# Optimization experiments

Hardware: AMD Instinct MI355X
Metric: run time of the kernel (lower is better)

Reference implementation:

```python
import jax, jax.numpy as jnp
import numpy as np

N_NODES = 500000
N_GRAPHS = 10000
NIN = 128
NOUT = 128
EPS = 1e-5


def setup_inputs() -> dict:
    key = jax.random.key(0)
    ks = jax.random.split(key, 10)
    x = jax.random.normal(ks[0], (N_NODES, NIN), dtype=jnp.float32)
    edge_index = jax.random.randint(ks[1], (2, 1000), 0, N_NODES, dtype=jnp.int64)
    edge_attr = jax.random.normal(ks[2], (1000, NIN), dtype=jnp.float32)
    batch = jnp.sort(jax.random.randint(ks[3], (N_NODES,), 0, N_GRAPHS, dtype=jnp.int64))
    s = 1.0 / np.sqrt(NIN)
    W_lin = jax.random.uniform(ks[4], (NIN, NIN), jnp.float32, -s, s)  # Linear(nin, nin, bias=False)
    bn_g = jnp.ones((NIN,), jnp.float32)
    bn_b = jnp.zeros((NIN,), jnp.float32)
    # MLP(nin, nout, nlayer=2, with_final_activation=False): Lin->BN->ReLU->Lin
    W1 = jax.random.uniform(ks[5], (NIN, NOUT), jnp.float32, -s, s)
    b1 = jax.random.uniform(ks[6], (NOUT,), jnp.float32, -s, s)
    bn1_g = jnp.ones((NOUT,), jnp.float32)
    bn1_b = jnp.zeros((NOUT,), jnp.float32)
    so = 1.0 / np.sqrt(NOUT)
    W2 = jax.random.uniform(ks[7], (NOUT, NOUT), jnp.float32, -so, so)
    b2 = jax.random.uniform(ks[8], (NOUT,), jnp.float32, -so, so)
    return {"x": x, "edge_index": edge_index, "edge_attr": edge_attr, "batch": batch,
            "W_lin": W_lin, "bn_g": bn_g, "bn_b": bn_b,
            "W1": W1, "b1": b1, "bn1_g": bn1_g, "bn1_b": bn1_b, "W2": W2, "b2": b2}


def _batchnorm(v, g, b):
    # training-mode BatchNorm1d: biased variance over dim 0
    mu = jnp.mean(v, axis=0, keepdims=True)
    var = jnp.mean(jnp.square(v - mu), axis=0, keepdims=True)
    return (v - mu) * jax.lax.rsqrt(var + EPS) * g + b


def reference(x, edge_index, edge_attr, batch, W_lin, bn_g, bn_b, W1, b1, bn1_g, bn1_b, W2, b2):
    # scatter-sum pooling: [num_graphs, nin]
    summation = jax.ops.segment_sum(x, batch, num_segments=N_GRAPHS)
    summation = summation @ W_lin.T if False else summation @ W_lin  # stored as [in,out]
    summation = jax.nn.relu(_batchnorm(summation, bn_g, bn_b))
    h = x + summation[batch]  # gather-broadcast add back to nodes
    # 2-layer MLP, no final activation
    h = jax.nn.relu(_batchnorm(h @ W1 + b1, bn1_g, bn1_b))
    return h @ W2 + b2
```

## Files before the change

### kernel.cpp

```cpp
#include <hip/hip_runtime.h>
#include <hip/hip_bf16.h>
#include <cstdint>
#include <cstddef>

#define NN 500000
#define NG 10000
#define F  128
#define EPSV 1e-5f

typedef __attribute__((ext_vector_type(8))) short short8;
typedef __attribute__((ext_vector_type(4))) float floatx4;

__device__ __forceinline__ short bfs(float f) {
    __hip_bfloat16 h = __float2bfloat16(f);
    union { __hip_bfloat16 h; unsigned short u; } c; c.h = h;
    return (short)c.u;
}
__device__ __forceinline__ int getb(const int* __restrict__ b, int i, int is64) {
    return is64 ? b[2 * i] : b[i];
}

__global__ void k_detect(const int* __restrict__ batch, int* __restrict__ flag) {
    __shared__ int nz;
    if (threadIdx.x == 0) nz = 0;
    __syncthreads();
    int j = 100001 + threadIdx.x * 1500;
    if (batch[j] != 0) atomicAdd(&nz, 1);
    __syncthreads();
    if (threadIdx.x == 0) flag[0] = (nz == 0) ? 1 : 0;
}

__global__ void k_bounds(const int* __restrict__ batch, int* __restrict__ gs, int* __restrict__ ge,
                         const int* __restrict__ flag) {
    int is64 = flag[0];
    int i = blockIdx.x * 256 + threadIdx.x;
    if (i >= NN) return;
    int b = getb(batch, i, is64);
    if (i == 0      || getb(batch, i - 1, is64) != b) gs[b] = i;
    if (i == NN - 1 || getb(batch, i + 1, is64) != b) ge[b] = i + 1;
}

__global__ void k_segsum(const float* __restrict__ x, const int* __restrict__ gs,
                         const int* __restrict__ ge, float* __restrict__ S,
                         unsigned short* __restrict__ xb) {
    __shared__ float red[8][128];
    int g = blockIdx.x;
    int s = gs[g], e = ge[g];
    int o = threadIdx.x & 31, rl = threadIdx.x >> 5;
    float acc[4] = {0.f, 0.f, 0.f, 0.f};
    for (int r = s + rl; r < e; r += 8) {
        float4 v = *reinterpret_cast<const float4*>(x + (size_t)r * F + o * 4);
        acc[0] += v.x; acc[1] += v.y; acc[2] += v.z; acc[3] += v.w;
        if (xb) {
            ushort4 bv;
            bv.x = (unsigned short)bfs(v.x); bv.y = (unsigned short)bfs(v.y);
            bv.z = (unsigned short)bfs(v.z); bv.w = (unsigned short)bfs(v.w);
            *reinterpret_cast<ushort4*>(xb + (size_t)r * F + o * 4) = bv;
        }
    }
#pragma unroll
    for (int j = 0; j < 4; j++) red[rl][o * 4 + j] = acc[j];
    __syncthreads();
    if (threadIdx.x < 128) {
        float ssum = 0.f;
#pragma unroll
        for (int rr = 0; rr < 8; rr++) ssum += red[rr][threadIdx.x];
        S[(size_t)g * F + threadIdx.x] = ssum;
    }
}

__global__ void k_wfrag(const float* __restrict__ W1, const float* __restrict__ W2,
                        unsigned short* __restrict__ W1f, unsigned short* __restrict__ W2f) {
    int i = blockIdx.x * 256 + threadIdx.x;
    int sel = i >> 14, j = i & 16383;
    int n = j >> 7, kk = j & 127;
    const float* W = sel ? W2 : W1;
    unsigned short* Wf = sel ? W2f : W1f;
    Wf[j] = (unsigned short)bfs(W[kk * F + n]);
}

__global__ void k_rowmm(const float* __restrict__ A, const float* __restrict__ W,
                        const float* __restrict__ bias, float* __restrict__ out, int hasBias) {
    int r = blockIdx.x * 2 + (threadIdx.x >> 7);
    int c = threadIdx.x & 127;
    const float* a = A + (size_t)r * F;
    float acc = hasBias ? bias[c] : 0.f;
#pragma unroll 4
    for (int k = 0; k < F; k++) acc += a[k] * W[k * F + c];
    out[(size_t)r * F + c] = acc;
}

__global__ void k_colstats(const float* __restrict__ T, float* __restrict__ sum, float* __restrict__ sumsq) {
    int f = threadIdx.x;
    int lo = blockIdx.x * 157;
    int hi = lo + 157; if (hi > NG) hi = NG;
    float s = 0.f, q = 0.f;
    for (int r = lo; r < hi; r++) { float v = T[(size_t)r * F + f]; s += v; q += v * v; }
    atomicAdd(&sum[f], s); atomicAdd(&sumsq[f], q);
}

__global__ void k_bn0(const float* __restrict__ sum, const float* __restrict__ sumsq,
                      const float* __restrict__ g, const float* __restrict__ b,
                      float* __restrict__ scale, float* __restrict__ shift) {
    int f = threadIdx.x;
    float mu  = sum[f] / (float)NG;
    float var = sumsq[f] / (float)NG - mu * mu;
    float rs  = rsqrtf(var + EPSV);
    float sc  = g[f] * rs;
    scale[f] = sc; shift[f] = b[f] - mu * sc;
}

__global__ void k_bnrelu(const float* __restrict__ T, const float* __restrict__ scale,
                         const float* __restrict__ shift, float* __restrict__ S2) {
    int e = (blockIdx.x * 256 + threadIdx.x) * 4;
    float4 t = *reinterpret_cast<const float4*>(T + e);
    int c = e & 127;
    float4 o;
    o.x = fmaxf(t.x * scale[c]     + shift[c],     0.f);
    o.y = fmaxf(t.y * scale[c + 1] + shift[c + 1], 0.f);
    o.z = fmaxf(t.z * scale[c + 2] + shift[c + 2], 0.f);
    o.w = fmaxf(t.w * scale[c + 3] + shift[c + 3], 0.f);
    *reinterpret_cast<float4*>(S2 + e) = o;
}

__device__ __forceinline__ short8 ld8bf(const float* __restrict__ p) {
    float4 f0 = *reinterpret_cast<const float4*>(p);
    float4 f1 = *reinterpret_cast<const float4*>(p + 4);
    short8 r;
    r[0] = bfs(f0.x); r[1] = bfs(f0.y); r[2] = bfs(f0.z); r[3] = bfs(f0.w);
    r[4] = bfs(f1.x); r[5] = bfs(f1.y); r[6] = bfs(f1.z); r[7] = bfs(f1.w);
    return r;
}


__global__ __launch_bounds__(256, 4)
void k_pass1(const unsigned short* __restrict__ xb, const int* __restrict__ batch,
             const unsigned short* __restrict__ W1f, const float* __restrict__ Z,
             float* __restrict__ partials, const int* __restrict__ flag) {
    const int is64 = flag[0];
    const int lane = threadIdx.x & 63;
    const int wave = threadIdx.x >> 6;
    const int wm = wave & 1, wn = wave >> 1;
    const int quad = lane >> 4, l16 = lane & 15;

    const unsigned short* wbase = W1f + ((wn * 64 + l16) * F + quad * 8);

    float su[4], sq[4];
#pragma unroll
    for (int nt = 0; nt < 4; nt++) { su[nt] = 0.f; sq[nt] = 0.f; }

    const int NT = (NN + 63) / 64;
    for (int tile = blockIdx.x; tile < NT; tile += gridDim.x) {
        int rb = tile * 64 + wm * 32;
        floatx4 acc[2][4];
#pragma unroll
        for (int mt = 0; mt < 2; mt++)
#pragma unroll
            for (int nt = 0; nt < 4; nt++) acc[mt][nt] = (floatx4){0.f, 0.f, 0.f, 0.f};

#pragma unroll
        for (int kt = 0; kt < 4; kt++) {
            short8 A[2];
#pragma unroll
            for (int mt = 0; mt < 2; mt++) {
                int r = rb + mt * 16 + l16; if (r >= NN) r = NN - 1;
                A[mt] = *reinterpret_cast<const short8*>(xb + (size_t)r * F + kt * 32 + quad * 8);
            }
#pragma unroll
            for (int nt = 0; nt < 4; nt++) {
                short8 B = *reinterpret_cast<const short8*>(wbase + nt * 16 * F + kt * 32);
#pragma unroll
                for (int mt = 0; mt < 2; mt++)
                    acc[mt][nt] = __builtin_amdgcn_mfma_f32_16x16x32_bf16(A[mt], B, acc[mt][nt], 0, 0, 0);
            }
        }

#pragma unroll
        for (int mt = 0; mt < 2; mt++)
#pragma unroll
            for (int reg = 0; reg < 4; reg++) {
                int r = rb + mt * 16 + quad * 4 + reg;
                bool valid = r < NN;
                int g = getb(batch, valid ? r : NN - 1, is64);
                const float* zr = Z + (size_t)g * F + wn * 64 + l16;
#pragma unroll
                for (int nt = 0; nt < 4; nt++) {
                    float u = acc[mt][nt][reg] + zr[nt * 16];
                    if (valid) { su[nt] += u; sq[nt] += u * u; }
                }
            }
    }

    float* ps = partials + (size_t)(blockIdx.x & 63) * 256;
#pragma unroll
    for (int nt = 0; nt < 4; nt++) {
        float s = su[nt], q = sq[nt];
        s += __shfl_xor(s, 16, 64); s += __shfl_xor(s, 32, 64);
        q += __shfl_xor(q, 16, 64); q += __shfl_xor(q, 32, 64);
        if (quad == 0) {
            int col = wn * 64 + nt * 16 + l16;
            atomicAdd(&ps[col], s);
            atomicAdd(&ps[128 + col], q);
        }
    }
}

__global__ void k_bn1(const float* __restrict__ partials, const float* __restrict__ g1,
                      const float* __restrict__ b1g, float* __restrict__ scale1,
                      float* __restrict__ shift1) {
    int f = threadIdx.x;
    float s = 0.f, q = 0.f;
    for (int t = 0; t < 64; t++) { s += partials[t * 256 + f]; q += partials[t * 256 + 128 + f]; }
    float mu  = s / (float)NN;
    float var = q / (float)NN - mu * mu;
    float rs  = rsqrtf(var + EPSV);
    float sc  = g1[f] * rs;
    scale1[f] = sc; shift1[f] = b1g[f] - mu * sc;
}

__global__ __launch_bounds__(256, 4)
void k_pass2(const unsigned short* __restrict__ xb, const int* __restrict__ batch,
             const unsigned short* W1f, const unsigned short* W2f,
             const float* __restrict__ Z, const float* __restrict__ scale1,
             const float* __restrict__ shift1, const float* __restrict__ b2,
             float* out, const int* __restrict__ flag) {
    __shared__ unsigned short h2[2][64][136];
    const int is64 = flag[0];
    const int lane = threadIdx.x & 63;
    const int wave = threadIdx.x >> 6;
    const int wm = wave & 1, wn = wave >> 1;
    const int quad = lane >> 4, l16 = lane & 15;

    float sc1[4], sh1[4], bb2[4];
#pragma unroll
    for (int nt = 0; nt < 4; nt++) {
        int n = wn * 64 + nt * 16 + l16;
        sc1[nt] = scale1[n]; sh1[nt] = shift1[n]; bb2[nt] = b2[n];
    }
    const unsigned short* w1base = W1f + ((wn * 64 + l16) * F + quad * 8);
    const unsigned short* w2base = W2f + ((wn * 64 + l16) * F + quad * 8);

    int buf = 0;
    const int NT = (NN + 63) / 64;
    for (int tile = blockIdx.x; tile < NT; tile += gridDim.x) {
        int rb = tile * 64 + wm * 32;
        floatx4 acc[2][4];
#pragma unroll
        for (int mt = 0; mt < 2; mt++)
#pragma unroll
            for (int nt = 0; nt < 4; nt++) acc[mt][nt] = (floatx4){0.f, 0.f, 0.f, 0.f};

#pragma unroll
        for (int kt = 0; kt < 4; kt++) {
            short8 A[2];
#pragma unroll
            for (int mt = 0; mt < 2; mt++) {
                int r = rb + mt * 16 + l16; if (r >= NN) r = NN - 1;
                A[mt] = *reinterpret_cast<const short8*>(xb + (size_t)r * F + kt * 32 + quad * 8);
            }
#pragma unroll
            for (int nt = 0; nt < 4; nt++) {
                short8 B = *reinterpret_cast<const short8*>(w1base + nt * 16 * F + kt * 32);
#pragma unroll
                for (int mt = 0; mt < 2; mt++)
                    acc[mt][nt] = __builtin_amdgcn_mfma_f32_16x16x32_bf16(A[mt], B, acc[mt][nt], 0, 0, 0);
            }
        }

#pragma unroll
        for (int mt = 0; mt < 2; mt++)
#pragma unroll
            for (int reg = 0; reg < 4; reg++) {
                int lr = wm * 32 + mt * 16 + quad * 4 + reg;
                int r = tile * 64 + lr; if (r >= NN) r = NN - 1;
                int g = getb(batch, r, is64);
                const float* zr = Z + (size_t)g * F + wn * 64 + l16;
#pragma unroll
                for (int nt = 0; nt < 4; nt++) {
                    float u = acc[mt][nt][reg] + zr[nt * 16];
                    float h = fmaxf(u * sc1[nt] + sh1[nt], 0.f);
                    h2[buf][lr][wn * 64 + nt * 16 + l16] = (unsigned short)bfs(h);
                }
            }
        __syncthreads();

        floatx4 acc2[2][4];
#pragma unroll
        for (int mt = 0; mt < 2; mt++)
#pragma unroll
            for (int nt = 0; nt < 4; nt++) acc2[mt][nt] = (floatx4){0.f, 0.f, 0.f, 0.f};
#pragma unroll
        for (int kt = 0; kt < 4; kt++) {
            short8 A2[2];
#pragma unroll
            for (int mt = 0; mt < 2; mt++)
                A2[mt] = *reinterpret_cast<const short8*>(&h2[buf][wm * 32 + mt * 16 + l16][kt * 32 + quad * 8]);
#pragma unroll
            for (int nt = 0; nt < 4; nt++) {
                short8 B = *reinterpret_cast<const short8*>(w2base + nt * 16 * F + kt * 32);
#pragma unroll
                for (int mt = 0; mt < 2; mt++)
                    acc2[mt][nt] = __builtin_amdgcn_mfma_f32_16x16x32_bf16(A2[mt], B, acc2[mt][nt], 0, 0, 0);
            }
        }

#pragma unroll
        for (int mt = 0; mt < 2; mt++)
#pragma unroll
            for (int reg = 0; reg < 4; reg++) {
                int r = rb + mt * 16 + quad * 4 + reg;
                if (r < NN) {
#pragma unroll
                    for (int nt = 0; nt < 4; nt++)
                        out[(size_t)r * F + wn * 64 + nt * 16 + l16] = acc2[mt][nt][reg] + bb2[nt];
                }
            }
        buf ^= 1;
    }
}


__global__ __launch_bounds__(256, 2)
void k_pass1_old(const float* __restrict__ x, const int* __restrict__ batch,
                 const float* __restrict__ W1, const float* __restrict__ Z,
                 float* __restrict__ partials, const int* __restrict__ flag) {
    const int is64 = flag[0];
    const int lane = threadIdx.x & 63;
    const int wave = threadIdx.x >> 6;
    const int wm = wave & 1, wn = wave >> 1;
    const int quad = lane >> 4, l16 = lane & 15;

    short8 Bf[4][4];
#pragma unroll
    for (int nt = 0; nt < 4; nt++) {
        int n = wn * 64 + nt * 16 + l16;
#pragma unroll
        for (int kt = 0; kt < 4; kt++)
#pragma unroll
            for (int j = 0; j < 8; j++)
                Bf[nt][kt][j] = bfs(W1[(kt * 32 + quad * 8 + j) * F + n]);
    }

    float su[4], sq[4];
#pragma unroll
    for (int nt = 0; nt < 4; nt++) { su[nt] = 0.f; sq[nt] = 0.f; }

    const int NT = (NN + 63) / 64;
    for (int tile = blockIdx.x; tile < NT; tile += gridDim.x) {
        int rb = tile * 64 + wm * 32;
        floatx4 acc[2][4];
#pragma unroll
        for (int mt = 0; mt < 2; mt++)
#pragma unroll
            for (int nt = 0; nt < 4; nt++) acc[mt][nt] = (floatx4){0.f, 0.f, 0.f, 0.f};

#pragma unroll
        for (int kt = 0; kt < 4; kt++) {
            short8 A[2];
#pragma unroll
            for (int mt = 0; mt < 2; mt++) {
                int r = rb + mt * 16 + l16; if (r >= NN) r = NN - 1;
                A[mt] = ld8bf(x + (size_t)r * F + kt * 32 + quad * 8);
            }
#pragma unroll
            for (int mt = 0; mt < 2; mt++)
#pragma unroll
                for (int nt = 0; nt < 4; nt++)
                    acc[mt][nt] = __builtin_amdgcn_mfma_f32_16x16x32_bf16(A[mt], Bf[nt][kt], acc[mt][nt], 0, 0, 0);
        }

#pragma unroll
        for (int mt = 0; mt < 2; mt++)
#pragma unroll
            for (int reg = 0; reg < 4; reg++) {
                int r = rb + mt * 16 + quad * 4 + reg;
                bool valid = r < NN;
                int g = getb(batch, valid ? r : NN - 1, is64);
                const float* zr = Z + (size_t)g * F + wn * 64 + l16;
#pragma unroll
                for (int nt = 0; nt < 4; nt++) {
                    float u = acc[mt][nt][reg] + zr[nt * 16];
                    if (valid) { su[nt] += u; sq[nt] += u * u; }
                }
            }
    }

    float* ps = partials + (size_t)(blockIdx.x & 63) * 256;
#pragma unroll
    for (int nt = 0; nt < 4; nt++) {
        float s = su[nt], q = sq[nt];
        s += __shfl_xor(s, 16, 64); s += __shfl_xor(s, 32, 64);
        q += __shfl_xor(q, 16, 64); q += __shfl_xor(q, 32, 64);
        if (quad == 0) {
            int col = wn * 64 + nt * 16 + l16;
            atomicAdd(&ps[col], s);
            atomicAdd(&ps[128 + col], q);
        }
    }
}

__global__ __launch_bounds__(256, 2)
void k_pass2_old(const float* __restrict__ x, const int* __restrict__ batch,
                 const float* __restrict__ W1, const float* __restrict__ W2,
                 const float* __restrict__ Z, const float* __restrict__ scale1,
                 const float* __restrict__ shift1, const float* __restrict__ b2,
                 float* __restrict__ out, const int* __restrict__ flag) {
    extern __shared__ unsigned short h2[];
    const int is64 = flag[0];
    const int lane = threadIdx.x & 63;
    const int wave = threadIdx.x >> 6;
    const int wm = wave & 1, wn = wave >> 1;
    const int quad = lane >> 4, l16 = lane & 15;

    short8 Bf1[4][4], Bf2[4][4];
    float sc1[4], sh1[4], bb2[4];
#pragma unroll
    for (int nt = 0; nt < 4; nt++) {
        int n = wn * 64 + nt * 16 + l16;
        sc1[nt] = scale1[n]; sh1[nt] = shift1[n]; bb2[nt] = b2[n];
#pragma unroll
        for (int kt = 0; kt < 4; kt++)
#pragma unroll
            for (int j = 0; j < 8; j++) {
                int k = kt * 32 + quad * 8 + j;
                Bf1[nt][kt][j] = bfs(W1[k * F + n]);
                Bf2[nt][kt][j] = bfs(W2[k * F + n]);
            }
    }

    const int NT = (NN + 63) / 64;
    for (int tile = blockIdx.x; tile < NT; tile += gridDim.x) {
        int rb = tile * 64 + wm * 32;
        floatx4 acc[2][4];
#pragma unroll
        for (int mt = 0; mt < 2; mt++)
#pragma unroll
            for (int nt = 0; nt < 4; nt++) acc[mt][nt] = (floatx4){0.f, 0.f, 0.f, 0.f};

#pragma unroll
        for (int kt = 0; kt < 4; kt++) {
            short8 A[2];
#pragma unroll
            for (int mt = 0; mt < 2; mt++) {
                int r = rb + mt * 16 + l16; if (r >= NN) r = NN - 1;
                A[mt] = ld8bf(x + (size_t)r * F + kt * 32 + quad * 8);
            }
#pragma unroll
            for (int mt = 0; mt < 2; mt++)
#pragma unroll
                for (int nt = 0; nt < 4; nt++)
                    acc[mt][nt] = __builtin_amdgcn_mfma_f32_16x16x32_bf16(A[mt], Bf1[nt][kt], acc[mt][nt], 0, 0, 0);
        }

        __syncthreads();
#pragma unroll
        for (int mt = 0; mt < 2; mt++)
#pragma unroll
            for (int reg = 0; reg < 4; reg++) {
                int lr = wm * 32 + mt * 16 + quad * 4 + reg;
                int r = tile * 64 + lr; if (r >= NN) r = NN - 1;
                int g = getb(batch, r, is64);
                const float* zr = Z + (size_t)g * F + wn * 64 + l16;
#pragma unroll
                for (int nt = 0; nt < 4; nt++) {
                    float u = acc[mt][nt][reg] + zr[nt * 16];
                    float h = fmaxf(u * sc1[nt] + sh1[nt], 0.f);
                    h2[lr * 136 + wn * 64 + nt * 16 + l16] = (unsigned short)bfs(h);
                }
            }
        __syncthreads();

        floatx4 acc2[2][4];
#pragma unroll
        for (int mt = 0; mt < 2; mt++)
#pragma unroll
            for (int nt = 0; nt < 4; nt++) acc2[mt][nt] = (floatx4){0.f, 0.f, 0.f, 0.f};
#pragma unroll
        for (int kt = 0; kt < 4; kt++) {
            short8 A2[2];
#pragma unroll
            for (int mt = 0; mt < 2; mt++)
                A2[mt] = *reinterpret_cast<const short8*>(&h2[(wm * 32 + mt * 16 + l16) * 136 + kt * 32 + quad * 8]);
#pragma unroll
            for (int mt = 0; mt < 2; mt++)
#pragma unroll
                for (int nt = 0; nt < 4; nt++)
                    acc2[mt][nt] = __builtin_amdgcn_mfma_f32_16x16x32_bf16(A2[mt], Bf2[nt][kt], acc2[mt][nt], 0, 0, 0);
        }

#pragma unroll
        for (int mt = 0; mt < 2; mt++)
#pragma unroll
            for (int reg = 0; reg < 4; reg++) {
                int r = rb + mt * 16 + quad * 4 + reg;
                if (r < NN) {
#pragma unroll
                    for (int nt = 0; nt < 4; nt++)
                        out[(size_t)r * F + wn * 64 + nt * 16 + l16] = acc2[mt][nt][reg] + bb2[nt];
                }
            }
    }
}

extern "C" void kernel_launch(void* const* d_in, const int* in_sizes, int n_in,
                              void* d_out, int out_size, void* d_ws, size_t ws_size,
                              hipStream_t stream) {
    const float* x    = (const float*)d_in[0];
    const int*   batch= (const int*)d_in[3];
    const float* Wl   = (const float*)d_in[4];
    const float* bng  = (const float*)d_in[5];
    const float* bnb  = (const float*)d_in[6];
    const float* W1   = (const float*)d_in[7];
    const float* b1   = (const float*)d_in[8];
    const float* bn1g = (const float*)d_in[9];
    const float* bn1b = (const float*)d_in[10];
    const float* W2   = (const float*)d_in[11];
    const float* b2   = (const float*)d_in[12];
    float* out = (float*)d_out;
    char* ws = (char*)d_ws;

    const size_t OFF_XB     = 0;
    const size_t OFF_W1F    = 128000000;
    const size_t OFF_W2F    = 128032768;
    const size_t OFF_S      = 128065536;
    const size_t OFF_T      = 133185536;
    const size_t OFF_GS     = 138305536;
    const size_t OFF_GE     = 138345536;
    const size_t OFF_SUM0   = 138385536;
    const size_t OFF_SUMSQ0 = 138386048;
    const size_t OFF_SCALE0 = 138386560;
    const size_t OFF_SHIFT0 = 138387072;
    const size_t OFF_PART   = 138387584;
    const size_t OFF_SCALE1 = 138453120;
    const size_t OFF_SHIFT1 = 138453632;
    const size_t OFF_FLAG   = 138454144;
    const size_t NEED       = 138454148;

    if (ws_size >= NEED) {
        unsigned short* xb  = (unsigned short*)(ws + OFF_XB);
        unsigned short* W1f = (unsigned short*)(ws + OFF_W1F);
        unsigned short* W2f = (unsigned short*)(ws + OFF_W2F);
        float* S        = (float*)(ws + OFF_S);
        float* T        = (float*)(ws + OFF_T);
        int*   gs       = (int*)  (ws + OFF_GS);
        int*   ge       = (int*)  (ws + OFF_GE);
        float* sum0     = (float*)(ws + OFF_SUM0);
        float* sumsq0   = (float*)(ws + OFF_SUMSQ0);
        float* scale0   = (float*)(ws + OFF_SCALE0);
        float* shift0   = (float*)(ws + OFF_SHIFT0);
        float* partials = (float*)(ws + OFF_PART);
        float* scale1   = (float*)(ws + OFF_SCALE1);
        float* shift1   = (float*)(ws + OFF_SHIFT1);
        int*   flag     = (int*)  (ws + OFF_FLAG);

        hipMemsetAsync(ws + OFF_GS, 0, NEED - OFF_GS, stream);

        k_detect <<<1, 256, 0, stream>>>(batch, flag);
        k_wfrag  <<<128, 256, 0, stream>>>(W1, W2, W1f, W2f);
        k_bounds <<<(NN + 255) / 256, 256, 0, stream>>>(batch, gs, ge, flag);
        k_segsum <<<NG, 256, 0, stream>>>(x, gs, ge, S, xb);
        k_rowmm  <<<NG / 2, 256, 0, stream>>>(S, Wl, nullptr, T, 0);
        k_colstats<<<64, 128, 0, stream>>>(T, sum0, sumsq0);
        k_bn0    <<<1, 128, 0, stream>>>(sum0, sumsq0, bng, bnb, scale0, shift0);
        k_bnrelu <<<NG * F / 1024, 256, 0, stream>>>(T, scale0, shift0, S);
        k_rowmm  <<<NG / 2, 256, 0, stream>>>(S, W1, b1, T, 1);
        k_pass1  <<<2048, 256, 0, stream>>>(xb, batch, W1f, T, partials, flag);
        k_bn1    <<<1, 128, 0, stream>>>(partials, bn1g, bn1b, scale1, shift1);
        k_pass2  <<<2048, 256, 0, stream>>>(xb, batch, W1f, W2f, T, scale1, shift1, b2, out, flag);
    } else {
        float* S        = (float*)(ws + 0);
        float* T        = (float*)(ws + 5120000);
        int*   gs       = (int*)  (ws + 10240000);
        int*   ge       = (int*)  (ws + 10280000);
        float* sum0     = (float*)(ws + 10320000);
        float* sumsq0   = (float*)(ws + 10320512);
        float* scale0   = (float*)(ws + 10321024);
        float* shift0   = (float*)(ws + 10321536);
        float* partials = (float*)(ws + 10322048);
        float* scale1   = (float*)(ws + 10387584);
        float* shift1   = (float*)(ws + 10388096);
        int*   flag     = (int*)  (ws + 10388608);

        hipMemsetAsync(ws + 10240000, 0, 147584, stream);

        k_detect <<<1, 256, 0, stream>>>(batch, flag);
        k_bounds <<<(NN + 255) / 256, 256, 0, stream>>>(batch, gs, ge, flag);
        k_segsum <<<NG, 256, 0, stream>>>(x, gs, ge, S, nullptr);
        k_rowmm  <<<NG / 2, 256, 0, stream>>>(S, Wl, nullptr, T, 0);
        k_colstats<<<64, 128, 0, stream>>>(T, sum0, sumsq0);
        k_bn0    <<<1, 128, 0, stream>>>(sum0, sumsq0, bng, bnb, scale0, shift0);
        k_bnrelu <<<NG * F / 1024, 256, 0, stream>>>(T, scale0, shift0, S);
        k_rowmm  <<<NG / 2, 256, 0, stream>>>(S, W1, b1, T, 1);
        k_pass1_old <<<2048, 256, 0, stream>>>(x, batch, W1, T, partials, flag);
        k_bn1    <<<1, 128, 0, stream>>>(partials, bn1g, bn1b, scale1, shift1);
        k_pass2_old <<<2048, 256, 64 * 136 * 2, stream>>>(x, batch, W1, W2, T, scale1, shift1, b2, out, flag);
    }
}
```

Measured before the change: 889.2 us.

## Keep W1 fragments in registers and stage swizzled W2 in LDS

```diff
diff --git a/kernel.cpp b/kernel.cpp
--- a/kernel.cpp
+++ b/kernel.cpp
@@ -133,7 +133,7 @@
 }
 
 
-__global__ __launch_bounds__(256, 4)
+__global__ __launch_bounds__(256, 3)
 void k_pass1(const unsigned short* __restrict__ xb, const int* __restrict__ batch,
              const unsigned short* __restrict__ W1f, const float* __restrict__ Z,
              float* __restrict__ partials, const int* __restrict__ flag) {
@@ -143,7 +143,13 @@
     const int wm = wave & 1, wn = wave >> 1;
     const int quad = lane >> 4, l16 = lane & 15;
 
-    const unsigned short* wbase = W1f + ((wn * 64 + l16) * F + quad * 8);
+    short8 Bf[4][4];
+#pragma unroll
+    for (int nt = 0; nt < 4; nt++)
+#pragma unroll
+        for (int kt = 0; kt < 4; kt++)
+            Bf[nt][kt] = *reinterpret_cast<const short8*>(
+                W1f + (wn * 64 + nt * 16 + l16) * F + kt * 32 + quad * 8);
 
     float su[4], sq[4];
 #pragma unroll
@@ -167,12 +173,10 @@
                 A[mt] = *reinterpret_cast<const short8*>(xb + (size_t)r * F + kt * 32 + quad * 8);
             }
 #pragma unroll
-            for (int nt = 0; nt < 4; nt++) {
-                short8 B = *reinterpret_cast<const short8*>(wbase + nt * 16 * F + kt * 32);
-#pragma unroll
-                for (int mt = 0; mt < 2; mt++)
-                    acc[mt][nt] = __builtin_amdgcn_mfma_f32_16x16x32_bf16(A[mt], B, acc[mt][nt], 0, 0, 0);
-            }
+            for (int mt = 0; mt < 2; mt++)
+#pragma unroll
+                for (int nt = 0; nt < 4; nt++)
+                    acc[mt][nt] = __builtin_amdgcn_mfma_f32_16x16x32_bf16(A[mt], Bf[nt][kt], acc[mt][nt], 0, 0, 0);
         }
 
 #pragma unroll
@@ -218,29 +222,45 @@
     scale1[f] = sc; shift1[f] = b1g[f] - mu * sc;
 }
 
-__global__ __launch_bounds__(256, 4)
+__global__ __launch_bounds__(256, 3)
 void k_pass2(const unsigned short* __restrict__ xb, const int* __restrict__ batch,
-             const unsigned short* W1f, const unsigned short* W2f,
+             const unsigned short* __restrict__ W1f, const unsigned short* __restrict__ W2f,
              const float* __restrict__ Z, const float* __restrict__ scale1,
              const float* __restrict__ shift1, const float* __restrict__ b2,
-             float* out, const int* __restrict__ flag) {
-    __shared__ unsigned short h2[2][64][136];
+             float* __restrict__ out, const int* __restrict__ flag) {
+    __shared__ unsigned short w2s[16384];
+    __shared__ unsigned short h2[64][136];
     const int is64 = flag[0];
     const int lane = threadIdx.x & 63;
     const int wave = threadIdx.x >> 6;
     const int wm = wave & 1, wn = wave >> 1;
     const int quad = lane >> 4, l16 = lane & 15;
 
+#pragma unroll
+    for (int c = 0; c < 8; c++) {
+        int j = threadIdx.x * 64 + c * 8;
+        int js = j ^ (((j >> 7) & 7) << 3);
+        *reinterpret_cast<short8*>(&w2s[js]) = *reinterpret_cast<const short8*>(W2f + j);
+    }
+
+    short8 Bf1[4][4];
+#pragma unroll
+    for (int nt = 0; nt < 4; nt++)
+#pragma unroll
+        for (int kt = 0; kt < 4; kt++)
+            Bf1[nt][kt] = *reinterpret_cast<const short8*>(
+                W1f + (wn * 64 + nt * 16 + l16) * F + kt * 32 + quad * 8);
+
     float sc1[4], sh1[4], bb2[4];
 #pragma unroll
     for (int nt = 0; nt < 4; nt++) {
         int n = wn * 64 + nt * 16 + l16;
         sc1[nt] = scale1[n]; sh1[nt] = shift1[n]; bb2[nt] = b2[n];
     }
-    const unsigned short* w1base = W1f + ((wn * 64 + l16) * F + quad * 8);
-    const unsigned short* w2base = W2f + ((wn * 64 + l16) * F + quad * 8);
-
-    int buf = 0;
+    const int jb2 = (wn * 64 + l16) * F + quad * 8;
+    const int X   = (l16 & 7) << 3;
+    __syncthreads();
+
     const int NT = (NN + 63) / 64;
     for (int tile = blockIdx.x; tile < NT; tile += gridDim.x) {
         int rb = tile * 64 + wm * 32;
@@ -259,14 +279,13 @@
                 A[mt] = *reinterpret_cast<const short8*>(xb + (size_t)r * F + kt * 32 + quad * 8);
             }
 #pragma unroll
-            for (int nt = 0; nt < 4; nt++) {
-                short8 B = *reinterpret_cast<const short8*>(w1base + nt * 16 * F + kt * 32);
-#pragma unroll
-                for (int mt = 0; mt < 2; mt++)
-                    acc[mt][nt] = __builtin_amdgcn_mfma_f32_16x16x32_bf16(A[mt], B, acc[mt][nt], 0, 0, 0);
-            }
-        }
-
+            for (int mt = 0; mt < 2; mt++)
+#pragma unroll
+                for (int nt = 0; nt < 4; nt++)
+                    acc[mt][nt] = __builtin_amdgcn_mfma_f32_16x16x32_bf16(A[mt], Bf1[nt][kt], acc[mt][nt], 0, 0, 0);
+        }
+
+        __syncthreads();
 #pragma unroll
         for (int mt = 0; mt < 2; mt++)
 #pragma unroll
@@ -279,7 +298,7 @@
                 for (int nt = 0; nt < 4; nt++) {
                     float u = acc[mt][nt][reg] + zr[nt * 16];
                     float h = fmaxf(u * sc1[nt] + sh1[nt], 0.f);
-                    h2[buf][lr][wn * 64 + nt * 16 + l16] = (unsigned short)bfs(h);
+                    h2[lr][wn * 64 + nt * 16 + l16] = (unsigned short)bfs(h);
                 }
             }
         __syncthreads();
@@ -294,10 +313,11 @@
             short8 A2[2];
 #pragma unroll
             for (int mt = 0; mt < 2; mt++)
-                A2[mt] = *reinterpret_cast<const short8*>(&h2[buf][wm * 32 + mt * 16 + l16][kt * 32 + quad * 8]);
+                A2[mt] = *reinterpret_cast<const short8*>(&h2[wm * 32 + mt * 16 + l16][kt * 32 + quad * 8]);
 #pragma unroll
             for (int nt = 0; nt < 4; nt++) {
-                short8 B = *reinterpret_cast<const short8*>(w2base + nt * 16 * F + kt * 32);
+                int jr = (jb2 + nt * 16 * F + kt * 32) ^ X;
+                short8 B = *reinterpret_cast<const short8*>(&w2s[jr]);
 #pragma unroll
                 for (int mt = 0; mt < 2; mt++)
                     acc2[mt][nt] = __builtin_amdgcn_mfma_f32_16x16x32_bf16(A2[mt], B, acc2[mt][nt], 0, 0, 0);
@@ -315,7 +335,6 @@
                         out[(size_t)r * F + wn * 64 + nt * 16 + l16] = acc2[mt][nt][reg] + bb2[nt];
                 }
             }
-        buf ^= 1;
     }
 }
 
@@ -405,7 +424,7 @@
                  const float* __restrict__ Z, const float* __restrict__ scale1,
                  const float* __restrict__ shift1, const float* __restrict__ b2,
                  float* __restrict__ out, const int* __restrict__ flag) {
-    extern __shared__ unsigned short h2[];
+    extern __shared__ unsigned short h2e[];
     const int is64 = flag[0];
     const int lane = threadIdx.x & 63;
     const int wave = threadIdx.x >> 6;
@@ -465,7 +484,7 @@
                 for (int nt = 0; nt < 4; nt++) {
                     float u = acc[mt][nt][reg] + zr[nt * 16];
                     float h = fmaxf(u * sc1[nt] + sh1[nt], 0.f);
-                    h2[lr * 136 + wn * 64 + nt * 16 + l16] = (unsigned short)bfs(h);
+                    h2e[lr * 136 + wn * 64 + nt * 16 + l16] = (unsigned short)bfs(h);
                 }
             }
         __syncthreads();
@@ -480,7 +499,7 @@
             short8 A2[2];
 #pragma unroll
             for (int mt = 0; mt < 2; mt++)
-                A2[mt] = *reinterpret_cast<const short8*>(&h2[(wm * 32 + mt * 16 + l16) * 136 + kt * 32 + quad * 8]);
+                A2[mt] = *reinterpret_cast<const short8*>(&h2e[(wm * 32 + mt * 16 + l16) * 136 + kt * 32 + quad * 8]);
 #pragma unroll
             for (int mt = 0; mt < 2; mt++)
 #pragma unroll
```

Measured after the change: 837.8 us. -5.8%, faster.
